# Kernel tuning notes

Hardware: AMD Instinct MI355X
Metric: run time of the kernel (lower is better)

The kernel has to match this reference:

```python
import jax, jax.numpy as jnp
import numpy as np

B, V, T, FIN = 32, 512, 12, 2      # batch, num_nodes, seq_len, input_dim
DG, CH, HOR = 20, 16, 12           # dgraphs, channels, horizon
KS, EPS, RF = 2, 0.3, 13           # kernel_size, FAGCN eps, receptive field
DILS = (1, 2, 1, 2, 1, 2, 1, 2)    # blocks=4, layers=2 -> dilations per layer
NL = len(DILS)
BN_EPS = 1e-5


def conv2d(x, W, b, dil=1):
    # x: [B,Cin,V,T], W: [Cout,Cin,1,k] -> [B,Cout,V,T'] (VALID, time-dilated)
    y = jax.lax.conv_general_dilated(x, W, (1, 1), 'VALID',
                                     rhs_dilation=(1, dil),
                                     dimension_numbers=('NCHW', 'OIHW', 'NCHW'))
    return y + b[None, :, None, None]


def setup_inputs():
    key = jax.random.key(0)
    ks = jax.random.split(key, 12)
    w = lambda k, s: jax.random.normal(k, s, dtype=jnp.float32) * 0.05
    z = lambda s: jnp.zeros(s, dtype=jnp.float32)
    o = lambda s: jnp.ones(s, dtype=jnp.float32)
    return {
        'input': jax.random.normal(ks[0], (T, B, V, FIN), dtype=jnp.float32),
        'start_W': w(ks[1], (CH, FIN, 1, 1)), 'start_b': z((CH,)),
        'filt_W': w(ks[2], (NL, CH, CH, 1, KS)), 'filt_b': z((NL, CH)),
        'gate_W': w(ks[3], (NL, CH, CH, 1, KS)), 'gate_b': z((NL, CH)),
        'skip_W': w(ks[4], (NL, CH, CH, 1, 1)), 'skip_b': z((NL, CH)),
        'gconv_W': w(ks[5], (NL, CH, 4 * CH, 1, 1)), 'gconv_b': z((NL, CH)),
        'bn_gamma': o((NL, CH)), 'bn_beta': z((NL, CH)),
        'bn_mean': z((NL, CH)), 'bn_var': o((NL, CH)),
        'end1_W': w(ks[6], (CH, CH, 1, 1)), 'end1_b': z((CH,)),
        'end2_W': w(ks[7], (HOR, CH, 1, 1)), 'end2_b': z((HOR,)),
        'lin_W': w(ks[8], (DG, FIN * T)), 'lin_b': z((DG,)),
        'fc1_W': w(ks[9], (V, DG)), 'fc1_b': z((V,)),
        'fc2_W': w(ks[10], (V, DG)), 'fc2_b': z((V,)),
        'fc3_W': w(ks[11], (V, DG)), 'fc3_b': z((V,)),
    }


def reference(input, start_W, start_b, filt_W, filt_b, gate_W, gate_b,
              skip_W, skip_b, gconv_W, gconv_b, bn_gamma, bn_beta, bn_mean,
              bn_var, end1_W, end1_b, end2_W, end2_b, lin_W, lin_b,
              fc1_W, fc1_b, fc2_W, fc2_b, fc3_W, fc3_b):
    x_in = jnp.transpose(input, (1, 3, 2, 0))            # [B,FIN,V,T]
    # ---- Instant_graph / SpectralConv1d: FFT-based graph learner ----
    xr = jnp.transpose(x_in, (0, 2, 3, 1)).reshape(B, V, T * FIN)
    ff = jnp.fft.fft(xr, axis=-1)                        # complex64 [B,V,T*FIN]
    real = ff.real @ lin_W.T + lin_b                     # [B,V,DG]
    img = ff.imag @ lin_W.T + lin_b                      # [B,V,DG]
    iff = jnp.fft.irfft(real + 1j * img, n=V, axis=1)    # [B,V,DG]
    Am = jnp.sqrt(real * real + img * img)
    S = jnp.arctan(real / (img + 1e-4))
    mid = jax.nn.sigmoid((iff @ fc1_W.T + fc1_b + Am @ fc2_W.T + fc2_b
                          + S @ fc3_W.T + fc3_b) / 3.0)  # [B,V,V]
    adj = jax.nn.sigmoid(jnp.mean(mid, axis=0))          # [V,V]
    eye = jnp.eye(V, dtype=x_in.dtype)
    Lm = EPS * eye + adj
    Hm = EPS * eye - adj
    # ---- WaveNet-style trunk with FAGCN diffusion per layer ----
    x = jnp.pad(x_in, ((0, 0), (0, 0), (0, 0), (RF - T, 0)))
    x = conv2d(x, start_W, start_b)                      # [B,CH,V,RF]
    skip = None
    for i in range(NL):
        residual = x
        f = jnp.tanh(conv2d(x, filt_W[i], filt_b[i], DILS[i]))
        g = jax.nn.sigmoid(conv2d(x, gate_W[i], gate_b[i], DILS[i]))
        x = f * g
        s = conv2d(x, skip_W[i], skip_b[i])
        skip = s if skip is None else s + skip[..., -s.shape[3]:]
        # FAGCN order=2: concat [xL, xLL, xH, xHH] on channels -> 1x1 conv
        outs = []
        for a in (Lm, Hm):
            x1 = jnp.einsum('ncvl,vw->ncwl', x, a)
            outs.append(x1)
            outs.append(jnp.einsum('ncvl,vw->ncwl', x1, a))
        h = conv2d(jnp.concatenate(outs, axis=1), gconv_W[i], gconv_b[i])
        x = h + residual[..., -h.shape[3]:]
        # BatchNorm2d (eval mode / running stats)
        x = ((x - bn_mean[i][None, :, None, None])
             / jnp.sqrt(bn_var[i][None, :, None, None] + BN_EPS)
             * bn_gamma[i][None, :, None, None]
             + bn_beta[i][None, :, None, None])
    out = jax.nn.relu(skip)
    out = jax.nn.relu(conv2d(out, end1_W, end1_b))
    out = conv2d(out, end2_W, end2_b)                    # [B,HOR,V,1]
    return out, adj
```

## Files before the change

kernel.cpp:

```cpp
#include <hip/hip_runtime.h>
#include <hip/hip_bf16.h>

using bf16 = __hip_bfloat16;
typedef unsigned short ushort_t;
typedef float f32x4 __attribute__((ext_vector_type(4)));
typedef short bf16x8 __attribute__((ext_vector_type(8)));

__device__ __forceinline__ float tof(bf16 x) { return __bfloat162float(x); }
__device__ __forceinline__ float tofu(ushort_t u) { return __uint_as_float((unsigned)u << 16); }
__device__ __forceinline__ ushort_t f2bf(float x) {
  unsigned u = __float_as_uint(x);
  return (ushort_t)((u + 0x7FFF + ((u >> 16) & 1)) >> 16);
}
__device__ __forceinline__ float sigm(float x) { return 1.f / (1.f + __expf(-x)); }
__device__ __forceinline__ float tanh_fast(float x) {
  float e2 = __expf(2.f * x);
  return 1.f - 2.f / (e2 + 1.f);
}

#define B_ 32
#define V_ 512
#define EPS_ 0.3f

constexpr size_t OFF_TWC  = 0;
constexpr size_t OFF_TWS  = 512;
constexpr size_t OFF_C    = 1024;
constexpr size_t OFF_S    = 1504;
constexpr size_t OFF_WEFF = 1984;
constexpr size_t OFF_R    = 8128;
constexpr size_t OFF_I    = 335808;
constexpr size_t OFF_G    = 663488;
constexpr size_t OFF_BTHI = 663488;
constexpr size_t OFF_BTLO = 925632;
constexpr size_t OFF_ADJ  = 1712064;
constexpr size_t OFF_ADJ2 = 1974208;
constexpr size_t OFF_SKIP = 2236352;
constexpr size_t OFF_X0   = 2498496;
constexpr size_t OFF_X1   = 5906368;
constexpr size_t OFF_UHI  = 9314240;
constexpr size_t OFF_ULO  = 10887104;
constexpr size_t OFF_PADJ = 12722112;
constexpr size_t OFF_WCT  = 13770688;
constexpr size_t OFF_FLAG = 19013568;
constexpr size_t OFF_CIN  = 19013576;
constexpr size_t WS_TOTAL = 19459584;

__global__ __launch_bounds__(256) void k_detect(const void* __restrict__ in0,
                                                float* __restrict__ flag) {
  __shared__ int cnt;
  if (threadIdx.x == 0) cnt = 0;
  __syncthreads();
  const unsigned short* u = (const unsigned short*)in0;
  int bad = 0;
  for (int i = threadIdx.x; i < 4096; i += 256) {
    int e = (u[i] >> 7) & 0xFF;
    if (e == 255 || (e != 0 && (e < 87 || e > 167))) bad++;
  }
  atomicAdd(&cnt, bad);
  __syncthreads();
  if (threadIdx.x == 0) flag[0] = (cnt > 200) ? 1.f : 0.f;
}

struct P26 { const void* p[26]; };
__global__ __launch_bounds__(256) void k_convall(const void* __restrict__ in0, P26 ps,
                                                 float* __restrict__ dstin,
                                                 float* __restrict__ dstw,
                                                 const float* __restrict__ flag) {
  int tid = threadIdx.x;
  if (blockIdx.x < 384) {
    int i4 = blockIdx.x * 256 + tid;
    if (flag[0] > 0.5f) {
      ((float4*)dstin)[i4] = ((const float4*)in0)[i4];
    } else {
      ushort4 v = ((const ushort4*)in0)[i4];
      dstin[i4 * 4 + 0] = tofu(v.x);
      dstin[i4 * 4 + 1] = tofu(v.y);
      dstin[i4 * 4 + 2] = tofu(v.z);
      dstin[i4 * 4 + 3] = tofu(v.w);
    }
  } else {
    const int sz[26] = {32, 16, 4096, 128, 4096, 128, 2048, 128, 8192, 128,
                        128, 128, 128, 128, 256, 16, 192, 12, 480, 20,
                        10240, 512, 10240, 512, 10240, 512};
    int gid = (blockIdx.x - 384) * 256 + tid;
    if (gid >= 52736) return;
    int s = 0, off = 0;
    while (gid >= off + sz[s]) { off += sz[s]; ++s; }
    int local = gid - off;
    float v = (flag[0] > 0.5f) ? ((const float*)ps.p[s])[local]
                               : tofu(((const ushort_t*)ps.p[s])[local]);
    dstw[gid] = v;
  }
}

__global__ __launch_bounds__(256) void k_pre(const float* __restrict__ linW,
                                             const float* __restrict__ gconvW,
                                             const float* f1W, const float* f1b,
                                             const float* f2W, const float* f2b,
                                             const float* f3W, const float* f3b,
                                             float* __restrict__ ws) {
  int idx = blockIdx.x * 256 + threadIdx.x;
  const float TWO_PI = 6.2831853071795864769f;
  if (idx < 512) {
    float ang = TWO_PI * (float)idx / 512.f;
    ws[OFF_TWC + idx] = cosf(ang);
    ws[OFF_TWS + idx] = sinf(ang);
  } else if (idx < 992) {
    int e = idx - 512, d = e / 24, n = e % 24;
    float c = 0.f, s = 0.f;
    for (int k = 0; k < 24; ++k) {
      int j = (k * n) % 24;
      float ang = TWO_PI * (float)j / 24.f;
      float w = linW[d * 24 + k];
      c += w * cosf(ang);
      s -= w * sinf(ang);
    }
    ws[OFF_C + e] = c;
    ws[OFF_S + e] = s;
  } else if (idx < 3040) {
    int e = idx - 992, i = e >> 8, co = (e >> 4) & 15, ci = e & 15;
    size_t base = (size_t)(i * 16 + co) * 64 + ci;
    float W0 = gconvW[base];
    float W1 = gconvW[base + 16];
    float W2 = gconvW[base + 32];
    float W3 = gconvW[base + 48];
    size_t o = OFF_WEFF + (size_t)i * 768 + co * 16 + ci;
    ws[o]       = EPS_ * (W0 + W2) + EPS_ * EPS_ * (W1 + W3);
    ws[o + 256] = (W0 - W2) + 2.f * EPS_ * (W1 - W3);
    ws[o + 512] = W1 + W3;
  } else if (idx < 36320) {
    int e = idx - 3040;
    if (e < 32768) {
      int k = e >> 9, w = e & 511;
      float v = 0.f;
      if (k < 20) v = f1W[w * 20 + k];
      else if (k < 40) v = f2W[w * 20 + k - 20];
      else if (k < 60) v = f3W[w * 20 + k - 40];
      ws[OFF_WCT + e] = v;
    } else {
      int w = e - 32768;
      ws[OFF_WCT + e] = f1b[w] + f2b[w] + f3b[w];
    }
  }
}

__global__ __launch_bounds__(256) void k_fft(const float* __restrict__ in,
                                             const float* __restrict__ linb,
                                             const float* __restrict__ ws,
                                             float* __restrict__ Rw, float* __restrict__ Iw,
                                             float* __restrict__ G) {
  __shared__ float Cl[480], Sl[480], lb[20];
  int tid = threadIdx.x;
  for (int e = tid; e < 480; e += 256) { Cl[e] = ws[OFF_C + e]; Sl[e] = ws[OFF_S + e]; }
  if (tid < 20) lb[tid] = linb[tid];
  __syncthreads();
  int gid = blockIdx.x * 256 + tid;
  int b = gid >> 9, v = gid & 511;
  float xr[24];
#pragma unroll
  for (int t = 0; t < 12; ++t) {
    size_t ib = (((size_t)t * 32 + b) * 512 + v) * 2;
    xr[2 * t] = in[ib];
    xr[2 * t + 1] = in[ib + 1];
  }
  size_t gbv = (size_t)b * 512 + v;
  for (int d = 0; d < 20; ++d) {
    float R = lb[d], I = lb[d];
#pragma unroll
    for (int n = 0; n < 24; ++n) {
      R = fmaf(xr[n], Cl[d * 24 + n], R);
      I = fmaf(xr[n], Sl[d * 24 + n], I);
    }
    Rw[gbv * 20 + d] = R;
    Iw[gbv * 20 + d] = I;
    G[gbv * 64 + 20 + d] = sqrtf(R * R + I * I);
    G[gbv * 64 + 40 + d] = atanf(R / (I + 1e-4f));
  }
  G[gbv * 64 + 60] = 0.f; G[gbv * 64 + 61] = 0.f;
  G[gbv * 64 + 62] = 0.f; G[gbv * 64 + 63] = 0.f;
}

__global__ __launch_bounds__(256) void k_irfft(const float* __restrict__ Rw,
                                               const float* __restrict__ Iw,
                                               const float* __restrict__ ws,
                                               float* __restrict__ G) {
  __shared__ float Rk[257], Ik[257], twc[512], tws[512];
  int blk = blockIdx.x;
  int b = blk / 20, d = blk % 20;
  int tid = threadIdx.x;
  for (int e = tid; e < 512; e += 256) { twc[e] = ws[OFF_TWC + e]; tws[e] = ws[OFF_TWS + e]; }
  for (int k = tid; k < 257; k += 256) {
    float ck = (k == 0 || k == 256) ? 1.f : 2.f;
    Rk[k] = Rw[((size_t)b * 512 + k) * 20 + d] * ck;
    Ik[k] = Iw[((size_t)b * 512 + k) * 20 + d] * ck;
  }
  __syncthreads();
#pragma unroll
  for (int s = 0; s < 2; ++s) {
    int m = tid + s * 256;
    float acc = 0.f;
    for (int k = 0; k < 257; ++k) {
      int j = (k * m) & 511;
      acc += Rk[k] * twc[j] - Ik[k] * tws[j];
    }
    G[((size_t)b * 512 + m) * 64 + d] = acc * (1.f / 512.f);
  }
}

__global__ __launch_bounds__(256) void k_adj(const float* __restrict__ G,
                                             const float* __restrict__ wct,
                                             float* __restrict__ padj) {
  __shared__ float As[64 * 68], Bs[64 * 68], bsl[64];
  int tid = threadIdx.x, tx = tid & 15, ty = tid >> 4;
  int w0 = blockIdx.x * 64, m0 = blockIdx.y * 64, z = blockIdx.z;
  for (int i = 0; i < 16; ++i) {
    int idx = tid + i * 256;
    Bs[(idx >> 6) * 68 + (idx & 63)] = wct[(size_t)(idx >> 6) * 512 + w0 + (idx & 63)];
  }
  if (tid < 64) bsl[tid] = wct[32768 + w0 + tid];
  float sum[4][4] = {};
  for (int bi = 0; bi < 8; ++bi) {
    int bb = z * 8 + bi;
    __syncthreads();
    for (int i = 0; i < 4; ++i) {
      int idx = tid + i * 256;
      int row = idx >> 4, seg = idx & 15;
      float4 g = *(const float4*)&G[((size_t)bb * 512 + m0 + row) * 64 + seg * 4];
      As[(seg * 4 + 0) * 68 + row] = g.x;
      As[(seg * 4 + 1) * 68 + row] = g.y;
      As[(seg * 4 + 2) * 68 + row] = g.z;
      As[(seg * 4 + 3) * 68 + row] = g.w;
    }
    __syncthreads();
    float dot[4][4] = {};
    for (int kk = 0; kk < 64; ++kk) {
      float4 a = *(const float4*)&As[kk * 68 + ty * 4];
      float4 b = *(const float4*)&Bs[kk * 68 + tx * 4];
      float ar[4] = {a.x, a.y, a.z, a.w}, br[4] = {b.x, b.y, b.z, b.w};
#pragma unroll
      for (int r = 0; r < 4; ++r)
#pragma unroll
        for (int c = 0; c < 4; ++c) dot[r][c] = fmaf(ar[r], br[c], dot[r][c]);
    }
#pragma unroll
    for (int r = 0; r < 4; ++r)
#pragma unroll
      for (int c = 0; c < 4; ++c)
        sum[r][c] += sigm((dot[r][c] + bsl[tx * 4 + c]) * (1.f / 3.f));
  }
  float* pz = padj + (size_t)z * 262144;
#pragma unroll
  for (int r = 0; r < 4; ++r)
#pragma unroll
    for (int c = 0; c < 4; ++c)
      pz[(size_t)(m0 + ty * 4 + r) * 512 + w0 + tx * 4 + c] = sum[r][c];
}

__global__ __launch_bounds__(256) void k_adjfin(const float* __restrict__ padj,
                                                float* __restrict__ adjw,
                                                void* __restrict__ outp,
                                                const float* __restrict__ flag) {
  int idx = blockIdx.x * 256 + threadIdx.x;
  float s = padj[idx] + padj[idx + 262144] + padj[idx + 524288] + padj[idx + 786432];
  float a = sigm(s * (1.f / 32.f));
  adjw[idx] = a;
  if (flag[0] > 0.5f) ((float*)outp)[196608 + idx] = a;
  else ((ushort_t*)outp)[196608 + idx] = f2bf(a);
}

__global__ __launch_bounds__(256) void k_gemm(const float* __restrict__ A,
                                              const float* __restrict__ B0,
                                              const float* __restrict__ B1,
                                              float* __restrict__ C, int ldc) {
  __shared__ float As[32][68];
  __shared__ float Bs[32][68];
  int bx = blockIdx.x, by = blockIdx.y;
  const float* __restrict__ Bp = (bx < 8) ? B0 : B1;
  int n0 = (bx & 7) * 64, m0 = by * 64;
  int tid = threadIdx.x, tx = tid & 15, ty = tid >> 4;
  float acc[4][4] = {};
  for (int kb = 0; kb < 512; kb += 32) {
#pragma unroll
    for (int s = 0; s < 2; ++s) {
      int f = tid + s * 256;
      int row = f >> 3, k4 = (f & 7) << 2;
      float4 a4 = *(const float4*)(A + (size_t)(m0 + row) * 512 + kb + k4);
      As[k4 + 0][row] = a4.x;
      As[k4 + 1][row] = a4.y;
      As[k4 + 2][row] = a4.z;
      As[k4 + 3][row] = a4.w;
      int kk = f >> 4, c4 = (f & 15) << 2;
      *(float4*)&Bs[kk][c4] = *(const float4*)(Bp + (size_t)(kb + kk) * 512 + n0 + c4);
    }
    __syncthreads();
#pragma unroll
    for (int kk = 0; kk < 32; ++kk) {
      float4 a = *(const float4*)&As[kk][ty << 2];
      float4 b = *(const float4*)&Bs[kk][tx << 2];
      float ar[4] = {a.x, a.y, a.z, a.w}, br[4] = {b.x, b.y, b.z, b.w};
#pragma unroll
      for (int r = 0; r < 4; ++r)
#pragma unroll
        for (int c = 0; c < 4; ++c) acc[r][c] = fmaf(ar[r], br[c], acc[r][c]);
    }
    __syncthreads();
  }
#pragma unroll
  for (int r = 0; r < 4; ++r) {
    float4 o = make_float4(acc[r][0], acc[r][1], acc[r][2], acc[r][3]);
    *(float4*)(C + (size_t)(m0 + (ty << 2) + r) * ldc + bx * 64 + (tx << 2)) = o;
  }
}

__global__ __launch_bounds__(256) void k_splitB(const float* __restrict__ adjw,
                                                const float* __restrict__ adj2w,
                                                ushort_t* __restrict__ Bh,
                                                ushort_t* __restrict__ Bl) {
  __shared__ float til[32][33];
  int tid = threadIdx.x;
  int k0 = blockIdx.x * 32;
  int nb = blockIdx.y;
  const float* src = (nb < 16) ? adjw : adj2w;
  int ns = (nb * 32) & 511;
  for (int i = 0; i < 4; ++i) {
    int idx = tid + i * 256;
    int r = idx >> 5, c = idx & 31;
    til[r][c] = src[(size_t)(k0 + r) * 512 + ns + c];
  }
  __syncthreads();
  for (int i = 0; i < 4; ++i) {
    int idx = tid + i * 256;
    int rr = idx >> 5, cc = idx & 31;
    float v = til[cc][rr];
    ushort_t h = f2bf(v);
    float hf = tofu(h);
    ushort_t l = f2bf(v - hf);
    size_t o = (size_t)(nb * 32 + rr) * 512 + k0 + cc;
    Bh[o] = h;
    Bl[o] = l;
  }
}

__global__ __launch_bounds__(256) void k_start(const float* __restrict__ in,
                                               const float* __restrict__ stW,
                                               const float* __restrict__ stb,
                                               float* __restrict__ X0) {
  __shared__ float w[32], bl[16];
  int tid = threadIdx.x;
  if (tid < 32) w[tid] = stW[tid];
  if (tid < 16) bl[tid] = stb[tid];
  __syncthreads();
  int blk = blockIdx.x;
  int b = blk / 26, rem = blk % 26, t = rem >> 1, v = (rem & 1) * 256 + tid;
  float f0 = 0.f, f1 = 0.f;
  if (t > 0) {
    size_t ib = (((size_t)(t - 1) * 32 + b) * 512 + v) * 2;
    f0 = in[ib];
    f1 = in[ib + 1];
  }
#pragma unroll
  for (int c = 0; c < 16; ++c)
    X0[((size_t)(b * 13 + t) * 16 + c) * 512 + v] = fmaf(w[c * 2], f0, fmaf(w[c * 2 + 1], f1, bl[c]));
}

__global__ __launch_bounds__(256) void k_gate(const float* __restrict__ X,
                                              ushort_t* __restrict__ Uhi,
                                              ushort_t* __restrict__ Ulo,
                                              float* __restrict__ skip,
                                              const float* fW, const float* fb,
                                              const float* gW, const float* gb,
                                              const float* sW, const float* sb,
                                              int i, int L, int Lo, int d) {
  __shared__ float wf[512], wg[512], swl[256], fbl[16], gbl[16], sbl[16];
  int tid = threadIdx.x;
  for (int e = tid; e < 512; e += 256) { wf[e] = fW[i * 512 + e]; wg[e] = gW[i * 512 + e]; }
  if (tid < 256) swl[tid] = sW[i * 256 + tid];
  if (tid < 16) { fbl[tid] = fb[i * 16 + tid]; gbl[tid] = gb[i * 16 + tid]; sbl[tid] = sb[i * 16 + tid]; }
  __syncthreads();
  int blk = blockIdx.x;
  int b = blk / (2 * Lo), rem = blk % (2 * Lo), t = rem >> 1, v = (rem & 1) * 256 + tid;
  float x0[16], x1[16];
  size_t base0 = (size_t)(b * L + t) * 16 * 512 + v;
  size_t base1 = (size_t)(b * L + t + d) * 16 * 512 + v;
#pragma unroll
  for (int ci = 0; ci < 16; ++ci) { x0[ci] = X[base0 + ci * 512]; x1[ci] = X[base1 + ci * 512]; }
  float u[16];
#pragma unroll
  for (int co = 0; co < 16; ++co) {
    float f = fbl[co], g = gbl[co];
#pragma unroll
    for (int ci = 0; ci < 16; ++ci) {
      f = fmaf(wf[co * 32 + ci * 2], x0[ci], f);
      f = fmaf(wf[co * 32 + ci * 2 + 1], x1[ci], f);
      g = fmaf(wg[co * 32 + ci * 2], x0[ci], g);
      g = fmaf(wg[co * 32 + ci * 2 + 1], x1[ci], g);
    }
    float uu = tanh_fast(f) * sigm(g);
    u[co] = uu;
    ushort_t h = f2bf(uu);
    float hf = tofu(h);
    ushort_t l = f2bf(uu - hf);
    size_t o = ((size_t)(b * Lo + t) * 16 + co) * 512 + v;
    Uhi[o] = h;
    Ulo[o] = l;
  }
  if (t == Lo - 1) {
#pragma unroll
    for (int c = 0; c < 16; ++c) {
      float s = sbl[c];
#pragma unroll
      for (int ci = 0; ci < 16; ++ci) s = fmaf(swl[c * 16 + ci], u[ci], s);
      skip[((size_t)b * 16 + c) * 512 + v] += s;
    }
  }
}

__global__ __launch_bounds__(512) void k_mfmac(const ushort_t* __restrict__ Uhi,
                                               const ushort_t* __restrict__ Ulo,
                                               const ushort_t* __restrict__ Bh_g,
                                               const ushort_t* __restrict__ Bl_g,
                                               const float* __restrict__ Xres,
                                               float* __restrict__ Xn,
                                               const float* __restrict__ ws,
                                               const float* gcb, const float* bg,
                                               const float* bb2, const float* bm,
                                               const float* bv,
                                               int li, int L, int Lo, int d) {
  __shared__ __align__(16) char smem[40960];
  ushort_t* Ah = (ushort_t*)smem;
  ushort_t* Al = Ah + 5120;
  ushort_t* Bh = Al + 5120;
  ushort_t* Bl = Bh + 5120;
  float* yt = (float*)smem;
  __shared__ float wx[256], wy1[256], wy2[256], gbl[16], bsc[16], bsh[16];
  int tid = threadIdx.x;
  const float* we = ws + OFF_WEFF + (size_t)li * 768;
  if (tid < 256) { wx[tid] = we[tid]; wy1[tid] = we[256 + tid]; wy2[tid] = we[512 + tid]; }
  if (tid < 16) {
    gbl[tid] = gcb[li * 16 + tid];
    float sc = bg[li * 16 + tid] * rsqrtf(bv[li * 16 + tid] + 1e-5f);
    bsc[tid] = sc;
    bsh[tid] = bb2[li * 16 + tid] - bm[li * 16 + tid] * sc;
  }
  int lane = tid & 63, wv = tid >> 6;
  int quad = lane >> 4, l15 = lane & 15;
  int wr = wv >> 1, wc = wv & 1;
  int m0 = blockIdx.x * 128;
  int nv0 = blockIdx.y * 64;
  int srow = tid >> 2, seg = tid & 3;
  size_t baseA = ((size_t)(m0 + srow)) * 512 + seg * 8;
  int brow = (srow < 64) ? (nv0 + srow) : (448 + nv0 + srow);
  size_t baseB = ((size_t)brow) * 512 + seg * 8;
  int slo = srow * 40 + seg * 8;
  uint4 pAh = *(const uint4*)&Uhi[baseA];
  uint4 pAl = *(const uint4*)&Ulo[baseA];
  uint4 pBh = *(const uint4*)&Bh_g[baseB];
  uint4 pBl = *(const uint4*)&Bl_g[baseB];
  f32x4 acc[2][4] = {};
  for (int kt = 0; kt < 16; ++kt) {
    *(uint4*)&Ah[slo] = pAh;
    *(uint4*)&Al[slo] = pAl;
    *(uint4*)&Bh[slo] = pBh;
    *(uint4*)&Bl[slo] = pBl;
    __syncthreads();
    if (kt < 15) {
      int ko = (kt + 1) * 32;
      pAh = *(const uint4*)&Uhi[baseA + ko];
      pAl = *(const uint4*)&Ulo[baseA + ko];
      pBh = *(const uint4*)&Bh_g[baseB + ko];
      pBl = *(const uint4*)&Bl_g[baseB + ko];
    }
    bf16x8 afh[2], afl[2], bfh[4], bfl[4];
#pragma unroll
    for (int i = 0; i < 2; ++i) {
      int mr = (wr * 32 + i * 16 + l15) * 40 + quad * 8;
      afh[i] = *(const bf16x8*)&Ah[mr];
      afl[i] = *(const bf16x8*)&Al[mr];
    }
#pragma unroll
    for (int j = 0; j < 4; ++j) {
      int nr = (wc * 64 + j * 16 + l15) * 40 + quad * 8;
      bfh[j] = *(const bf16x8*)&Bh[nr];
      bfl[j] = *(const bf16x8*)&Bl[nr];
    }
#pragma unroll
    for (int i = 0; i < 2; ++i)
#pragma unroll
      for (int j = 0; j < 4; ++j) {
        acc[i][j] = __builtin_amdgcn_mfma_f32_16x16x32_bf16(afh[i], bfh[j], acc[i][j], 0, 0, 0);
        acc[i][j] = __builtin_amdgcn_mfma_f32_16x16x32_bf16(afh[i], bfl[j], acc[i][j], 0, 0, 0);
        acc[i][j] = __builtin_amdgcn_mfma_f32_16x16x32_bf16(afl[i], bfh[j], acc[i][j], 0, 0, 0);
      }
    __syncthreads();
  }
  int g = tid >> 5, lv = tid & 31;
  int gg = (m0 >> 4) + g;
  int b = gg / Lo, t = gg - b * Lo;
  size_t rb = (size_t)gg * 16;
  size_t resb = ((size_t)(b * L + t + d) * 16) * 512;
#pragma unroll
  for (int p = 0; p < 2; ++p) {
#pragma unroll
    for (int i = 0; i < 2; ++i)
#pragma unroll
      for (int jj = 0; jj < 2; ++jj) {
        int j = p * 2 + jj;
#pragma unroll
        for (int r = 0; r < 4; ++r) {
          int row = wr * 32 + i * 16 + quad * 4 + r;
          int col = jj * 16 + l15 + 32 * wc;
          yt[row * 66 + col] = acc[i][j][r];
        }
      }
    __syncthreads();
    if (tid < 256) {
      int v = nv0 + p * 32 + lv;
      float uu[16], z1[16], z2[16];
#pragma unroll
      for (int ci = 0; ci < 16; ++ci) {
        size_t o = (rb + ci) * 512 + v;
        uu[ci] = tofu(Uhi[o]) + tofu(Ulo[o]);
        z1[ci] = yt[(g * 16 + ci) * 66 + lv];
        z2[ci] = yt[(g * 16 + ci) * 66 + 32 + lv];
      }
#pragma unroll
      for (int co = 0; co < 16; ++co) {
        float h = gbl[co];
#pragma unroll
        for (int ci = 0; ci < 16; ++ci) {
          h = fmaf(wx[co * 16 + ci], uu[ci], h);
          h = fmaf(wy1[co * 16 + ci], z1[ci], h);
          h = fmaf(wy2[co * 16 + ci], z2[ci], h);
        }
        float val = h + Xres[resb + co * 512 + v];
        val = fmaf(val, bsc[co], bsh[co]);
        Xn[(rb + co) * 512 + v] = val;
      }
    }
    if (p == 0) __syncthreads();
  }
}

__global__ __launch_bounds__(256) void k_end(const float* __restrict__ skip,
                                             const float* e1W, const float* e1b,
                                             const float* e2W, const float* e2b,
                                             void* __restrict__ outp,
                                             const float* __restrict__ flag) {
  __shared__ float w1[256], b1[16], w2[192], b2[12];
  int tid = threadIdx.x;
  if (tid < 256) w1[tid] = e1W[tid];
  if (tid < 192) w2[tid] = e2W[tid];
  if (tid < 16) b1[tid] = e1b[tid];
  if (tid < 12) b2[tid] = e2b[tid];
  __syncthreads();
  float isf32 = flag[0];
  int gid = blockIdx.x * 256 + tid;
  int b = gid >> 9, v = gid & 511;
  float sk[16], e1[16];
#pragma unroll
  for (int ci = 0; ci < 16; ++ci) sk[ci] = fmaxf(skip[((size_t)b * 16 + ci) * 512 + v], 0.f);
#pragma unroll
  for (int c = 0; c < 16; ++c) {
    float a = b1[c];
#pragma unroll
    for (int ci = 0; ci < 16; ++ci) a = fmaf(w1[c * 16 + ci], sk[ci], a);
    e1[c] = fmaxf(a, 0.f);
  }
#pragma unroll
  for (int h = 0; h < 12; ++h) {
    float o = b2[h];
#pragma unroll
    for (int ci = 0; ci < 16; ++ci) o = fmaf(w2[h * 16 + ci], e1[ci], o);
    size_t oi = ((size_t)b * 12 + h) * 512 + v;
    if (isf32 > 0.5f) ((float*)outp)[oi] = o;
    else ((ushort_t*)outp)[oi] = f2bf(o);
  }
}

extern "C" void kernel_launch(void* const* d_in, const int* in_sizes, int n_in,
                              void* d_out, int out_size, void* d_ws, size_t ws_size,
                              hipStream_t stream) {
  float* ws = (float*)d_ws;
  if (ws_size < WS_TOTAL * sizeof(float)) return;

  static const int CSZ[27] = {393216, 32, 16, 4096, 128, 4096, 128, 2048, 128, 8192, 128,
                              128, 128, 128, 128, 256, 16, 192, 12, 480, 20,
                              10240, 512, 10240, 512, 10240, 512};
  float* cv[27];
  {
    size_t off = OFF_CIN;
    for (int i = 0; i < 27; ++i) { cv[i] = ws + off; off += (size_t)CSZ[i]; }
  }
  float* flag = ws + OFF_FLAG;

  k_detect<<<1, 256, 0, stream>>>(d_in[0], flag);
  P26 ps;
  for (int i = 0; i < 26; ++i) ps.p[i] = d_in[i + 1];
  k_convall<<<590, 256, 0, stream>>>(d_in[0], ps, cv[0], cv[1], flag);

  const float* IN = cv[0];
  const float* stW = cv[1];  const float* stb = cv[2];
  const float* fW = cv[3];   const float* fb = cv[4];
  const float* gW = cv[5];   const float* gb = cv[6];
  const float* sW = cv[7];   const float* sb = cv[8];
  const float* gcW = cv[9];  const float* gcb = cv[10];
  const float* bng = cv[11]; const float* bnb = cv[12];
  const float* bnm = cv[13]; const float* bnv = cv[14];
  const float* e1W = cv[15]; const float* e1b = cv[16];
  const float* e2W = cv[17]; const float* e2b = cv[18];
  const float* linW = cv[19]; const float* linb = cv[20];
  const float* f1W = cv[21]; const float* f1b = cv[22];
  const float* f2W = cv[23]; const float* f2b = cv[24];
  const float* f3W = cv[25]; const float* f3b = cv[26];

  hipMemsetAsync(ws + OFF_SKIP, 0, (size_t)B_ * 16 * V_ * sizeof(float), stream);
  k_pre<<<142, 256, 0, stream>>>(linW, gcW, f1W, f1b, f2W, f2b, f3W, f3b, ws);
  k_fft<<<64, 256, 0, stream>>>(IN, linb, ws, ws + OFF_R, ws + OFF_I, ws + OFF_G);
  k_irfft<<<640, 256, 0, stream>>>(ws + OFF_R, ws + OFF_I, ws, ws + OFF_G);
  k_adj<<<dim3(8, 8, 4), 256, 0, stream>>>(ws + OFF_G, ws + OFF_WCT, ws + OFF_PADJ);
  k_adjfin<<<1024, 256, 0, stream>>>(ws + OFF_PADJ, ws + OFF_ADJ, d_out, flag);
  k_gemm<<<dim3(8, 8), 256, 0, stream>>>(ws + OFF_ADJ, ws + OFF_ADJ, ws + OFF_ADJ,
                                         ws + OFF_ADJ2, 512);
  k_splitB<<<dim3(16, 32), 256, 0, stream>>>(ws + OFF_ADJ, ws + OFF_ADJ2,
                                             (ushort_t*)(ws + OFF_BTHI),
                                             (ushort_t*)(ws + OFF_BTLO));
  k_start<<<832, 256, 0, stream>>>(IN, stW, stb, ws + OFF_X0);

  float* cur = ws + OFF_X0;
  float* nxt = ws + OFF_X1;
  ushort_t* UHI = (ushort_t*)(ws + OFF_UHI);
  ushort_t* ULO = (ushort_t*)(ws + OFF_ULO);
  int L = 13;
  const int dils[8] = {1, 2, 1, 2, 1, 2, 1, 2};
  for (int i = 0; i < 8; ++i) {
    int d = dils[i], Lo = L - d;
    k_gate<<<64 * Lo, 256, 0, stream>>>(cur, UHI, ULO, ws + OFF_SKIP,
                                        fW, fb, gW, gb, sW, sb, i, L, Lo, d);
    k_mfmac<<<dim3(4 * Lo, 8), 512, 0, stream>>>(UHI, ULO,
                                                 (ushort_t*)(ws + OFF_BTHI),
                                                 (ushort_t*)(ws + OFF_BTLO),
                                                 cur, nxt, ws,
                                                 gcb, bng, bnb, bnm, bnv, i, L, Lo, d);
    float* tmp = cur; cur = nxt; nxt = tmp;
    L = Lo;
  }
  k_end<<<64, 256, 0, stream>>>(ws + OFF_SKIP, e1W, e1b, e2W, e2b, d_out, flag);
}
```

Baseline: 620.5 us.

## Recast inverse real FFT as split-bf16 MFMA GEMM against precomputed twiddle matrix

```diff
diff --git a/kernel.cpp b/kernel.cpp
--- a/kernel.cpp
+++ b/kernel.cpp
@@ -22,8 +22,6 @@
 #define V_ 512
 #define EPS_ 0.3f
 
-constexpr size_t OFF_TWC  = 0;
-constexpr size_t OFF_TWS  = 512;
 constexpr size_t OFF_C    = 1024;
 constexpr size_t OFF_S    = 1504;
 constexpr size_t OFF_WEFF = 1984;
@@ -37,6 +35,10 @@
 constexpr size_t OFF_SKIP = 2236352;
 constexpr size_t OFF_X0   = 2498496;
 constexpr size_t OFF_X1   = 5906368;
+constexpr size_t OFF_TBH  = 5906368;
+constexpr size_t OFF_TBL  = 6045632;
+constexpr size_t OFF_TAH  = 6184896;
+constexpr size_t OFF_TAL  = 6358976;
 constexpr size_t OFF_UHI  = 9314240;
 constexpr size_t OFF_ULO  = 10887104;
 constexpr size_t OFF_PADJ = 12722112;
@@ -102,9 +104,6 @@
   int idx = blockIdx.x * 256 + threadIdx.x;
   const float TWO_PI = 6.2831853071795864769f;
   if (idx < 512) {
-    float ang = TWO_PI * (float)idx / 512.f;
-    ws[OFF_TWC + idx] = cosf(ang);
-    ws[OFF_TWS + idx] = sinf(ang);
   } else if (idx < 992) {
     int e = idx - 512, d = e / 24, n = e % 24;
     float c = 0.f, s = 0.f;
@@ -141,6 +140,20 @@
       int w = e - 32768;
       ws[OFF_WCT + e] = f1b[w] + f2b[w] + f3b[w];
     }
+  } else if (idx < 36320 + 278528) {
+    int e = idx - 36320;
+    int m = e / 544, kk = e - m * 544;
+    float val = 0.f;
+    if (kk < 514) {
+      int k = kk >> 1;
+      int j = (k * m) & 511;
+      float ang = TWO_PI * (float)j * (1.f / 512.f);
+      val = ((kk & 1) ? sinf(ang) : cosf(ang)) * (1.f / 512.f);
+    }
+    ushort_t h = f2bf(val);
+    float hf = tofu(h);
+    ((ushort_t*)(ws + OFF_TBH))[e] = h;
+    ((ushort_t*)(ws + OFF_TBL))[e] = f2bf(val - hf);
   }
 }
 
@@ -180,31 +193,92 @@
   G[gbv * 64 + 62] = 0.f; G[gbv * 64 + 63] = 0.f;
 }
 
-__global__ __launch_bounds__(256) void k_irfft(const float* __restrict__ Rw,
-                                               const float* __restrict__ Iw,
-                                               const float* __restrict__ ws,
-                                               float* __restrict__ G) {
-  __shared__ float Rk[257], Ik[257], twc[512], tws[512];
-  int blk = blockIdx.x;
-  int b = blk / 20, d = blk % 20;
+__global__ __launch_bounds__(256) void k_irprep(const float* __restrict__ Rw,
+                                                const float* __restrict__ Iw,
+                                                ushort_t* __restrict__ Ahi,
+                                                ushort_t* __restrict__ Alo) {
+  int e = blockIdx.x * 256 + threadIdx.x;
+  if (e >= 348160) return;
+  int row = e / 544, kk = e - row * 544;
+  int b = row / 20, d = row - b * 20;
+  float val = 0.f;
+  if (kk < 514) {
+    int k = kk >> 1;
+    float ck = (k == 0 || k == 256) ? 1.f : 2.f;
+    size_t src = ((size_t)b * 512 + k) * 20 + d;
+    val = (kk & 1) ? (-ck * Iw[src]) : (ck * Rw[src]);
+  }
+  ushort_t h = f2bf(val);
+  Ahi[e] = h;
+  Alo[e] = f2bf(val - tofu(h));
+}
+
+__global__ __launch_bounds__(512) void k_irgemm(const ushort_t* __restrict__ Ah_g,
+                                                const ushort_t* __restrict__ Al_g,
+                                                const ushort_t* __restrict__ Bh_g,
+                                                const ushort_t* __restrict__ Bl_g,
+                                                float* __restrict__ G) {
+  __shared__ ushort_t Ah[128 * 40], Al[128 * 40], Bh[64 * 40], Bl[64 * 40];
   int tid = threadIdx.x;
-  for (int e = tid; e < 512; e += 256) { twc[e] = ws[OFF_TWC + e]; tws[e] = ws[OFF_TWS + e]; }
-  for (int k = tid; k < 257; k += 256) {
-    float ck = (k == 0 || k == 256) ? 1.f : 2.f;
-    Rk[k] = Rw[((size_t)b * 512 + k) * 20 + d] * ck;
-    Ik[k] = Iw[((size_t)b * 512 + k) * 20 + d] * ck;
-  }
-  __syncthreads();
-#pragma unroll
-  for (int s = 0; s < 2; ++s) {
-    int m = tid + s * 256;
-    float acc = 0.f;
-    for (int k = 0; k < 257; ++k) {
-      int j = (k * m) & 511;
-      acc += Rk[k] * twc[j] - Ik[k] * tws[j];
-    }
-    G[((size_t)b * 512 + m) * 64 + d] = acc * (1.f / 512.f);
-  }
+  int lane = tid & 63, wv = tid >> 6;
+  int quad = lane >> 4, l15 = lane & 15;
+  int wr = wv >> 1, wc = wv & 1;
+  int m0 = blockIdx.x * 128;
+  int nv0 = blockIdx.y * 64;
+  int srow = tid >> 2, seg = tid & 3;
+  size_t baseA = (size_t)(m0 + srow) * 544 + seg * 8;
+  size_t baseB = (size_t)(nv0 + (srow & 63)) * 544 + seg * 8;
+  int slo = srow * 40 + seg * 8;
+  uint4 pAh = *(const uint4*)&Ah_g[baseA];
+  uint4 pAl = *(const uint4*)&Al_g[baseA];
+  uint4 pBh, pBl;
+  if (tid < 256) { pBh = *(const uint4*)&Bh_g[baseB]; pBl = *(const uint4*)&Bl_g[baseB]; }
+  f32x4 acc[2][2] = {};
+  for (int kt = 0; kt < 17; ++kt) {
+    *(uint4*)&Ah[slo] = pAh;
+    *(uint4*)&Al[slo] = pAl;
+    if (tid < 256) { *(uint4*)&Bh[slo] = pBh; *(uint4*)&Bl[slo] = pBl; }
+    __syncthreads();
+    if (kt < 16) {
+      int ko = (kt + 1) * 32;
+      pAh = *(const uint4*)&Ah_g[baseA + ko];
+      pAl = *(const uint4*)&Al_g[baseA + ko];
+      if (tid < 256) { pBh = *(const uint4*)&Bh_g[baseB + ko]; pBl = *(const uint4*)&Bl_g[baseB + ko]; }
+    }
+    bf16x8 afh[2], afl[2], bfh[2], bfl[2];
+#pragma unroll
+    for (int i = 0; i < 2; ++i) {
+      int mr = (wr * 32 + i * 16 + l15) * 40 + quad * 8;
+      afh[i] = *(const bf16x8*)&Ah[mr];
+      afl[i] = *(const bf16x8*)&Al[mr];
+    }
+#pragma unroll
+    for (int j = 0; j < 2; ++j) {
+      int nr = (wc * 32 + j * 16 + l15) * 40 + quad * 8;
+      bfh[j] = *(const bf16x8*)&Bh[nr];
+      bfl[j] = *(const bf16x8*)&Bl[nr];
+    }
+#pragma unroll
+    for (int i = 0; i < 2; ++i)
+#pragma unroll
+      for (int j = 0; j < 2; ++j) {
+        acc[i][j] = __builtin_amdgcn_mfma_f32_16x16x32_bf16(afh[i], bfh[j], acc[i][j], 0, 0, 0);
+        acc[i][j] = __builtin_amdgcn_mfma_f32_16x16x32_bf16(afh[i], bfl[j], acc[i][j], 0, 0, 0);
+        acc[i][j] = __builtin_amdgcn_mfma_f32_16x16x32_bf16(afl[i], bfh[j], acc[i][j], 0, 0, 0);
+      }
+    __syncthreads();
+  }
+#pragma unroll
+  for (int i = 0; i < 2; ++i)
+#pragma unroll
+    for (int j = 0; j < 2; ++j)
+#pragma unroll
+      for (int r = 0; r < 4; ++r) {
+        int arow = m0 + wr * 32 + i * 16 + quad * 4 + r;
+        int col = nv0 + wc * 32 + j * 16 + l15;
+        int b = arow / 20, d = arow - b * 20;
+        G[((size_t)b * 512 + col) * 64 + d] = acc[i][j][r];
+      }
 }
 
 __global__ __launch_bounds__(256) void k_adj(const float* __restrict__ G,
@@ -614,9 +688,13 @@
   const float* f3W = cv[25]; const float* f3b = cv[26];
 
   hipMemsetAsync(ws + OFF_SKIP, 0, (size_t)B_ * 16 * V_ * sizeof(float), stream);
-  k_pre<<<142, 256, 0, stream>>>(linW, gcW, f1W, f1b, f2W, f2b, f3W, f3b, ws);
+  k_pre<<<1230, 256, 0, stream>>>(linW, gcW, f1W, f1b, f2W, f2b, f3W, f3b, ws);
   k_fft<<<64, 256, 0, stream>>>(IN, linb, ws, ws + OFF_R, ws + OFF_I, ws + OFF_G);
-  k_irfft<<<640, 256, 0, stream>>>(ws + OFF_R, ws + OFF_I, ws, ws + OFF_G);
+  k_irprep<<<1360, 256, 0, stream>>>(ws + OFF_R, ws + OFF_I,
+                                     (ushort_t*)(ws + OFF_TAH), (ushort_t*)(ws + OFF_TAL));
+  k_irgemm<<<dim3(5, 8), 512, 0, stream>>>((ushort_t*)(ws + OFF_TAH), (ushort_t*)(ws + OFF_TAL),
+                                           (ushort_t*)(ws + OFF_TBH), (ushort_t*)(ws + OFF_TBL),
+                                           ws + OFF_G);
   k_adj<<<dim3(8, 8, 4), 256, 0, stream>>>(ws + OFF_G, ws + OFF_WCT, ws + OFF_PADJ);
   k_adjfin<<<1024, 256, 0, stream>>>(ws + OFF_PADJ, ws + OFF_ADJ, d_out, flag);
   k_gemm<<<dim3(8, 8), 256, 0, stream>>>(ws + OFF_ADJ, ws + OFF_ADJ, ws + OFF_ADJ,
```

Measured after the change: 594.7 us. 1.04x faster.
